# Kernel tuning notes

Measured on AMD Instinct MI355X. Metric: run time of the kernel, lower is better.

Reference implementation:

```python
import jax, jax.numpy as jnp
import numpy as np

EPS = 1e-5
L = 512
P1 = 64  # patch_num + 1
B = 512
H = 2048


def layernorm2d(x, g, b):
    # LayerNorm over the last two dims [P1, L]
    mu = jnp.mean(x, axis=(-2, -1), keepdims=True)
    var = jnp.mean(jnp.square(x - mu), axis=(-2, -1), keepdims=True)
    return (x - mu) * jax.lax.rsqrt(var + EPS) * g + b


def freq_filter(x, w):
    # rfft(x) * rfft(w) then irfft, all with ortho normalization
    X = jnp.fft.rfft(x, axis=-1, norm='ortho')          # [B, P1, L//2+1]
    W = jnp.fft.rfft(w, axis=-1, norm='ortho')          # [1, L//2+1]
    return jnp.fft.irfft(X * W, n=L, axis=-1, norm='ortho')


def setup_inputs() -> dict:
    key = jax.random.key(0)
    ks = jax.random.split(key, 4)
    x = jax.random.normal(ks[0], (B, P1, L), dtype=jnp.float32)
    w = 0.02 * jax.random.normal(ks[1], (1, L), dtype=jnp.float32)
    w1 = jax.random.normal(ks[2], (L, H), dtype=jnp.float32) * (1.0 / np.sqrt(L))
    b1 = jnp.zeros((H,), jnp.float32)
    w2 = jax.random.normal(ks[3], (H, L), dtype=jnp.float32) * (1.0 / np.sqrt(H))
    b2 = jnp.zeros((L,), jnp.float32)
    return {
        'x': x, 'w': w,
        'ln1_w': jnp.ones((P1, L), jnp.float32), 'ln1_b': jnp.zeros((P1, L), jnp.float32),
        'ln2_w': jnp.ones((P1, L), jnp.float32), 'ln2_b': jnp.zeros((P1, L), jnp.float32),
        'w1': w1, 'b1': b1, 'w2': w2, 'b2': b2,
    }


def reference(x, w, ln1_w, ln1_b, ln2_w, ln2_b, w1, b1, w2, b2):
    res = x
    h = layernorm2d(x, ln1_w, ln1_b)
    h = freq_filter(h, w)
    # dropout is identity in inference
    h = layernorm2d(h, ln2_w, ln2_b)
    # PositionwiseFeedForward: Linear -> ReLU -> (dropout) -> Linear
    h = jax.nn.relu(jnp.einsum('bpl,lh->bph', h, w1) + b1)
    h = jnp.einsum('bph,hl->bpl', h, w2) + b2
    return h + res
```

## Files before the change

### kernel.cpp

```cpp
#include <hip/hip_runtime.h>

typedef __bf16  bf16x8 __attribute__((ext_vector_type(8)));
typedef float   f32x4  __attribute__((ext_vector_type(4)));
typedef unsigned short u16;

__device__ __forceinline__ u16 f2bf(float f) {
  union { float f; unsigned u32; } c; c.f = f;
  unsigned r = c.u32 + 0x7fffu + ((c.u32 >> 16) & 1u);
  return (u16)(r >> 16);
}
__device__ __forceinline__ float bf2f(u16 u) {
  union { unsigned u32; float f; } c; c.u32 = (unsigned)u << 16; return c.f;
}

__device__ __forceinline__ void async16(const void* g, void* l) {
  __builtin_amdgcn_global_load_lds(
      (const __attribute__((address_space(1))) unsigned*)g,
      (__attribute__((address_space(3))) unsigned*)l, 16, 0, 0);
}

__global__ __launch_bounds__(256) void build_ct(const float* __restrict__ w,
                                                u16* __restrict__ ct) {
  int idx = blockIdx.x * 256 + threadIdx.x;
  int n = idx >> 9, k = idx & 511;
  float v = w[(n - k) & 511] * 0.04419417382415922f;
  ct[idx] = f2bf(v);
}

__global__ __launch_bounds__(256) void transpose_w(const float* __restrict__ in,
                                                   u16* __restrict__ out,
                                                   int R, int C) {
  __shared__ float tile[32][33];
  int bx = blockIdx.x * 32;
  int by = blockIdx.y * 32;
  int tx = threadIdx.x & 31, ty = threadIdx.x >> 5;
#pragma unroll
  for (int r = ty; r < 32; r += 8)
    tile[r][tx] = in[(size_t)(by + r) * C + bx + tx];
  __syncthreads();
#pragma unroll
  for (int r = ty; r < 32; r += 8)
    out[(size_t)(bx + r) * R + by + tx] = f2bf(tile[tx][r]);
}

__global__ __launch_bounds__(512, 2) void ln_f32(const float* __restrict__ x,
                                                 const float* __restrict__ g,
                                                 const float* __restrict__ beta,
                                                 u16* __restrict__ out) {
  const int tid = threadIdx.x;
  const size_t base = (size_t)blockIdx.x * 32768;
  float4 v[16];
  float s = 0.f, ss = 0.f;
#pragma unroll
  for (int j = 0; j < 16; ++j) {
    v[j] = *(const float4*)(x + base + tid * 4 + j * 2048);
    s  += v[j].x + v[j].y + v[j].z + v[j].w;
    ss += v[j].x * v[j].x + v[j].y * v[j].y + v[j].z * v[j].z + v[j].w * v[j].w;
  }
#pragma unroll
  for (int off = 32; off > 0; off >>= 1) {
    s += __shfl_down(s, off, 64);
    ss += __shfl_down(ss, off, 64);
  }
  __shared__ float red[16];
  int wave = tid >> 6, lane = tid & 63;
  if (lane == 0) { red[wave] = s; red[8 + wave] = ss; }
  __syncthreads();
  float S = 0.f, SS = 0.f;
#pragma unroll
  for (int wv = 0; wv < 8; ++wv) { S += red[wv]; SS += red[8 + wv]; }
  const float inv = 1.0f / 32768.0f;
  float mu = S * inv;
  float rs = rsqrtf(SS * inv - mu * mu + 1e-5f);
#pragma unroll
  for (int j = 0; j < 16; ++j) {
    const int i = tid * 4 + j * 2048;
    float4 gv = *(const float4*)(g + i);
    float4 bv = *(const float4*)(beta + i);
    uint2 o;
    o.x = (unsigned)f2bf((v[j].x - mu) * rs * gv.x + bv.x) |
          ((unsigned)f2bf((v[j].y - mu) * rs * gv.y + bv.y) << 16);
    o.y = (unsigned)f2bf((v[j].z - mu) * rs * gv.z + bv.z) |
          ((unsigned)f2bf((v[j].w - mu) * rs * gv.w + bv.w) << 16);
    *(uint2*)(out + base + i) = o;
  }
}

__global__ __launch_bounds__(512, 2) void ln_bf16(const u16* __restrict__ x,
                                                  const float* __restrict__ g,
                                                  const float* __restrict__ beta,
                                                  u16* __restrict__ out) {
  const int tid = threadIdx.x;
  const size_t base = (size_t)blockIdx.x * 32768;
  uint4 v[8];
  float s = 0.f, ss = 0.f;
#pragma unroll
  for (int j = 0; j < 8; ++j) {
    v[j] = *(const uint4*)(x + base + tid * 8 + j * 4096);
    const unsigned* a = &v[j].x;
#pragma unroll
    for (int t = 0; t < 4; ++t) {
      float lo = bf2f((u16)(a[t] & 0xffff)), hi = bf2f((u16)(a[t] >> 16));
      s += lo + hi; ss += lo * lo + hi * hi;
    }
  }
#pragma unroll
  for (int off = 32; off > 0; off >>= 1) {
    s += __shfl_down(s, off, 64);
    ss += __shfl_down(ss, off, 64);
  }
  __shared__ float red[16];
  int wave = tid >> 6, lane = tid & 63;
  if (lane == 0) { red[wave] = s; red[8 + wave] = ss; }
  __syncthreads();
  float S = 0.f, SS = 0.f;
#pragma unroll
  for (int wv = 0; wv < 8; ++wv) { S += red[wv]; SS += red[8 + wv]; }
  const float inv = 1.0f / 32768.0f;
  float mu = S * inv;
  float rs = rsqrtf(SS * inv - mu * mu + 1e-5f);
#pragma unroll
  for (int j = 0; j < 8; ++j) {
    const int i = tid * 8 + j * 4096;
    const unsigned* a = &v[j].x;
    uint4 o;
    unsigned* ov = &o.x;
#pragma unroll
    for (int t = 0; t < 4; ++t) {
      float lo = bf2f((u16)(a[t] & 0xffff)), hi = bf2f((u16)(a[t] >> 16));
      float4 gv2; float2 bv2;
      float glo = g[i + 2 * t], ghi = g[i + 2 * t + 1];
      float blo = beta[i + 2 * t], bhi = beta[i + 2 * t + 1];
      (void)gv2; (void)bv2;
      ov[t] = (unsigned)f2bf((lo - mu) * rs * glo + blo) |
              ((unsigned)f2bf((hi - mu) * rs * ghi + bhi) << 16);
    }
    *(uint4*)(out + base + i) = o;
  }
}

template <int MODE>
__global__ __launch_bounds__(256, 4) void gemm_bt(
    const u16* __restrict__ A, const u16* __restrict__ Bt,
    const float* __restrict__ bias, const float* __restrict__ resid,
    float* __restrict__ Cf, u16* __restrict__ Cb, int M, int N, int K) {
  __shared__ u16 As[128 * 64];
  __shared__ u16 Bs[128 * 64];
  const int tid = threadIdx.x;
  const int wave = tid >> 6, lane = tid & 63;
  const int quad = lane >> 4, l16 = lane & 15;
  const int wm = (wave >> 1) * 64, wn = (wave & 1) * 64;
  const int m0 = blockIdx.x * 128, n0 = blockIdx.y * 128;

  f32x4 acc[4][4];
#pragma unroll
  for (int i = 0; i < 4; ++i)
#pragma unroll
    for (int j = 0; j < 4; ++j) acc[i][j] = (f32x4){0.f, 0.f, 0.f, 0.f};

  const int rbase = tid >> 3;
  const int slot  = tid & 7;
  const int gcol  = (slot ^ (rbase & 7)) * 8;
  const int lofs  = tid * 8;

  const u16* ag = A + (size_t)(m0 + rbase) * K + gcol;
  const u16* bg = Bt + (size_t)(n0 + rbase) * K + gcol;
  const int swr = (l16 & 7);

  for (int k0 = 0; k0 < K; k0 += 64) {
    __syncthreads();
#pragma unroll
    for (int j = 0; j < 4; ++j) {
      async16(ag + (size_t)(32 * j) * K + k0, &As[lofs + j * 2048]);
      async16(bg + (size_t)(32 * j) * K + k0, &Bs[lofs + j * 2048]);
    }
    __syncthreads();
#pragma unroll
    for (int h = 0; h < 2; ++h) {
      const int sw = (((h << 2) + quad) ^ swr) * 8;
      bf16x8 af[4], bfr[4];
#pragma unroll
      for (int i = 0; i < 4; ++i)
        af[i] = *(const bf16x8*)&As[(wm + i * 16 + l16) * 64 + sw];
#pragma unroll
      for (int j = 0; j < 4; ++j)
        bfr[j] = *(const bf16x8*)&Bs[(wn + j * 16 + l16) * 64 + sw];
#pragma unroll
      for (int i = 0; i < 4; ++i)
#pragma unroll
        for (int j = 0; j < 4; ++j)
          acc[i][j] = __builtin_amdgcn_mfma_f32_16x16x32_bf16(af[i], bfr[j],
                                                              acc[i][j], 0, 0, 0);
    }
  }

#pragma unroll
  for (int j = 0; j < 4; ++j) {
    const int col = n0 + wn + j * 16 + l16;
    float bj = 0.f;
    if (MODE >= 1) bj = bias[col];
#pragma unroll
    for (int i = 0; i < 4; ++i) {
      const int rowb = m0 + wm + i * 16 + quad * 4;
#pragma unroll
      for (int r = 0; r < 4; ++r) {
        float v = acc[i][j][r] + bj;
        if (MODE == 1) v = fmaxf(v, 0.f);
        size_t idx = (size_t)(rowb + r) * N + col;
        if (MODE == 2) { v += resid[idx]; Cf[idx] = v; }
        else           Cb[idx] = f2bf(v);
      }
    }
  }
}

extern "C" void kernel_launch(void* const* d_in, const int* in_sizes, int n_in,
                              void* d_out, int out_size, void* d_ws,
                              size_t ws_size, hipStream_t stream) {
  const float* x    = (const float*)d_in[0];
  const float* w    = (const float*)d_in[1];
  const float* ln1w = (const float*)d_in[2];
  const float* ln1b = (const float*)d_in[3];
  const float* ln2w = (const float*)d_in[4];
  const float* ln2b = (const float*)d_in[5];
  const float* w1   = (const float*)d_in[6];
  const float* b1   = (const float*)d_in[7];
  const float* w2   = (const float*)d_in[8];
  const float* b2   = (const float*)d_in[9];
  float* out = (float*)d_out;

  char* ws = (char*)d_ws;
  u16*   y   = (u16*)(ws);
  u16*   h1  = (u16*)(ws);
  u16*   h2  = (u16*)(ws + 33554432);
  u16*   h3  = (u16*)(ws + 134217728);
  u16*   ct  = (u16*)(ws + 167772160);
  u16*   w1t = (u16*)(ws + 168296448);
  u16*   w2t = (u16*)(ws + 170393600);

  build_ct<<<1024, 256, 0, stream>>>(w, ct);
  transpose_w<<<dim3(64, 16), 256, 0, stream>>>(w1, w1t, 512, 2048);
  transpose_w<<<dim3(16, 64), 256, 0, stream>>>(w2, w2t, 2048, 512);

  ln_f32<<<512, 512, 0, stream>>>(x, ln1w, ln1b, h1);
  gemm_bt<0><<<dim3(256, 4), 256, 0, stream>>>(h1, ct, nullptr, nullptr,
                                               nullptr, h2, 32768, 512, 512);
  ln_bf16<<<512, 512, 0, stream>>>(h2, ln2w, ln2b, h3);
  gemm_bt<1><<<dim3(256, 16), 256, 0, stream>>>(h3, w1t, b1, nullptr,
                                                nullptr, y, 32768, 2048, 512);
  gemm_bt<2><<<dim3(256, 4), 256, 0, stream>>>(y, w2t, b2, x,
                                               out, nullptr, 32768, 512, 2048);
}
```

Baseline: 389.7 us.

## Double-buffer GEMM K-tiles with async LDS prefetch and merge weight-prep kernels

The bf16 MFMA GEMM now uses two 128x32 LDS buffers per operand. It prefetches the next K-slice with global_load_lds while computing on the current one, needing a single barrier per iteration instead of two. The LDS swizzle is adapted to 32-wide rows. The three weight-preparation kernels (circulant build and two transposes) are merged into one launch to cut launch overhead, and the LayerNorm epilogue is tidied. The trade-off is twice as many loop iterations with a smaller K step and a new swizzle pattern that could change LDS bank behaviour.

```diff
diff --git a/kernel.cpp b/kernel.cpp
--- a/kernel.cpp
+++ b/kernel.cpp
@@ -19,21 +19,31 @@
       (__attribute__((address_space(3))) unsigned*)l, 16, 0, 0);
 }
 
-__global__ __launch_bounds__(256) void build_ct(const float* __restrict__ w,
-                                                u16* __restrict__ ct) {
-  int idx = blockIdx.x * 256 + threadIdx.x;
-  int n = idx >> 9, k = idx & 511;
-  float v = w[(n - k) & 511] * 0.04419417382415922f;
-  ct[idx] = f2bf(v);
-}
-
-__global__ __launch_bounds__(256) void transpose_w(const float* __restrict__ in,
-                                                   u16* __restrict__ out,
-                                                   int R, int C) {
+__global__ __launch_bounds__(256) void prep(const float* __restrict__ w,
+                                            u16* __restrict__ ct,
+                                            const float* __restrict__ w1,
+                                            u16* __restrict__ w1t,
+                                            const float* __restrict__ w2,
+                                            u16* __restrict__ w2t) {
   __shared__ float tile[32][33];
-  int bx = blockIdx.x * 32;
-  int by = blockIdx.y * 32;
-  int tx = threadIdx.x & 31, ty = threadIdx.x >> 5;
+  const int b = blockIdx.x;
+  const int tid = threadIdx.x;
+  if (b < 1024) {
+    int idx = b * 256 + tid;
+    int n = idx >> 9, k = idx & 511;
+    ct[idx] = f2bf(w[(n - k) & 511] * 0.04419417382415922f);
+    return;
+  }
+  const float* in;  u16* out;  int R, C, bx, by;
+  if (b < 2048) {
+    in = w1; out = w1t; R = 512; C = 2048;
+    bx = (b - 1024) & 63; by = (b - 1024) >> 6;
+  } else {
+    in = w2; out = w2t; R = 2048; C = 512;
+    bx = (b - 2048) & 15; by = (b - 2048) >> 4;
+  }
+  bx *= 32; by *= 32;
+  int tx = tid & 31, ty = tid >> 5;
 #pragma unroll
   for (int r = ty; r < 32; r += 8)
     tile[r][tx] = in[(size_t)(by + r) * C + bx + tx];
@@ -128,12 +138,9 @@
 #pragma unroll
     for (int t = 0; t < 4; ++t) {
       float lo = bf2f((u16)(a[t] & 0xffff)), hi = bf2f((u16)(a[t] >> 16));
-      float4 gv2; float2 bv2;
-      float glo = g[i + 2 * t], ghi = g[i + 2 * t + 1];
-      float blo = beta[i + 2 * t], bhi = beta[i + 2 * t + 1];
-      (void)gv2; (void)bv2;
-      ov[t] = (unsigned)f2bf((lo - mu) * rs * glo + blo) |
-              ((unsigned)f2bf((hi - mu) * rs * ghi + bhi) << 16);
+      ov[t] = (unsigned)f2bf((lo - mu) * rs * g[i + 2 * t] + beta[i + 2 * t]) |
+              ((unsigned)f2bf((hi - mu) * rs * g[i + 2 * t + 1] +
+                              beta[i + 2 * t + 1]) << 16);
     }
     *(uint4*)(out + base + i) = o;
   }
@@ -144,8 +151,8 @@
     const u16* __restrict__ A, const u16* __restrict__ Bt,
     const float* __restrict__ bias, const float* __restrict__ resid,
     float* __restrict__ Cf, u16* __restrict__ Cb, int M, int N, int K) {
-  __shared__ u16 As[128 * 64];
-  __shared__ u16 Bs[128 * 64];
+  __shared__ u16 As[2][128 * 32];
+  __shared__ u16 Bs[2][128 * 32];
   const int tid = threadIdx.x;
   const int wave = tid >> 6, lane = tid & 63;
   const int quad = lane >> 4, l16 = lane & 15;
@@ -158,40 +165,47 @@
 #pragma unroll
     for (int j = 0; j < 4; ++j) acc[i][j] = (f32x4){0.f, 0.f, 0.f, 0.f};
 
-  const int rbase = tid >> 3;
-  const int slot  = tid & 7;
-  const int gcol  = (slot ^ (rbase & 7)) * 8;
-  const int lofs  = tid * 8;
-
-  const u16* ag = A + (size_t)(m0 + rbase) * K + gcol;
-  const u16* bg = Bt + (size_t)(n0 + rbase) * K + gcol;
-  const int swr = (l16 & 7);
-
-  for (int k0 = 0; k0 < K; k0 += 64) {
+  const int carow = tid >> 2;
+  const int chunk = tid & 3;
+  const int gcol = (chunk ^ ((carow >> 1) & 3)) * 8;
+  const int lslot0 = carow * 32 + chunk * 8;
+  const int lslot1 = (carow + 64) * 32 + chunk * 8;
+  const int sw = (quad ^ ((l16 >> 1) & 3)) * 8;
+
+  const u16* ag0 = A + (size_t)(m0 + carow) * K + gcol;
+  const u16* ag1 = A + (size_t)(m0 + carow + 64) * K + gcol;
+  const u16* bg0 = Bt + (size_t)(n0 + carow) * K + gcol;
+  const u16* bg1 = Bt + (size_t)(n0 + carow + 64) * K + gcol;
+
+  const int nT = K >> 5;
+  async16(ag0, &As[0][lslot0]);
+  async16(ag1, &As[0][lslot1]);
+  async16(bg0, &Bs[0][lslot0]);
+  async16(bg1, &Bs[0][lslot1]);
+
+  for (int t = 0; t < nT; ++t) {
     __syncthreads();
-#pragma unroll
-    for (int j = 0; j < 4; ++j) {
-      async16(ag + (size_t)(32 * j) * K + k0, &As[lofs + j * 2048]);
-      async16(bg + (size_t)(32 * j) * K + k0, &Bs[lofs + j * 2048]);
-    }
-    __syncthreads();
-#pragma unroll
-    for (int h = 0; h < 2; ++h) {
-      const int sw = (((h << 2) + quad) ^ swr) * 8;
-      bf16x8 af[4], bfr[4];
-#pragma unroll
-      for (int i = 0; i < 4; ++i)
-        af[i] = *(const bf16x8*)&As[(wm + i * 16 + l16) * 64 + sw];
+    if (t + 1 < nT) {
+      const int k = (t + 1) << 5, pb = (t + 1) & 1;
+      async16(ag0 + k, &As[pb][lslot0]);
+      async16(ag1 + k, &As[pb][lslot1]);
+      async16(bg0 + k, &Bs[pb][lslot0]);
+      async16(bg1 + k, &Bs[pb][lslot1]);
+    }
+    const int cb = t & 1;
+    bf16x8 af[4], bfr[4];
+#pragma unroll
+    for (int i = 0; i < 4; ++i)
+      af[i] = *(const bf16x8*)&As[cb][(wm + i * 16 + l16) * 32 + sw];
+#pragma unroll
+    for (int j = 0; j < 4; ++j)
+      bfr[j] = *(const bf16x8*)&Bs[cb][(wn + j * 16 + l16) * 32 + sw];
+#pragma unroll
+    for (int i = 0; i < 4; ++i)
 #pragma unroll
       for (int j = 0; j < 4; ++j)
-        bfr[j] = *(const bf16x8*)&Bs[(wn + j * 16 + l16) * 64 + sw];
-#pragma unroll
-      for (int i = 0; i < 4; ++i)
-#pragma unroll
-        for (int j = 0; j < 4; ++j)
-          acc[i][j] = __builtin_amdgcn_mfma_f32_16x16x32_bf16(af[i], bfr[j],
-                                                              acc[i][j], 0, 0, 0);
-    }
+        acc[i][j] = __builtin_amdgcn_mfma_f32_16x16x32_bf16(af[i], bfr[j],
+                                                            acc[i][j], 0, 0, 0);
   }
 
 #pragma unroll
@@ -238,9 +252,7 @@
   u16*   w1t = (u16*)(ws + 168296448);
   u16*   w2t = (u16*)(ws + 170393600);
 
-  build_ct<<<1024, 256, 0, stream>>>(w, ct);
-  transpose_w<<<dim3(64, 16), 256, 0, stream>>>(w1, w1t, 512, 2048);
-  transpose_w<<<dim3(16, 64), 256, 0, stream>>>(w2, w2t, 2048, 512);
+  prep<<<3072, 256, 0, stream>>>(w, ct, w1, w1t, w2, w2t);
 
   ln_f32<<<512, 512, 0, stream>>>(x, ln1w, ln1b, h1);
   gemm_bt<0><<<dim3(256, 4), 256, 0, stream>>>(h1, ct, nullptr, nullptr,
```

New measurement: 398.1 us. 2.2% more time.
